# Optimization experiments

Hardware: AMD Instinct MI355X
Metric: run time of the kernel (lower is better)

## Reference

```python
import jax, jax.numpy as jnp
import numpy as np

N_NODES = 80000
N_EDGES = 1280000
N_GRAPHS = 256
NEG_SLOPE = 0.2


def _edge_softmax(alpha, dst, n):
    # PyG softmax over incoming edges per target node, with 1e-16 eps
    m = jax.ops.segment_max(alpha, dst, num_segments=n)          # [N,H]
    e = jnp.exp(alpha - m[dst])
    s = jax.ops.segment_sum(e, dst, num_segments=n)              # [N,H]
    return e / (s[dst] + 1e-16)


def _gat_layer(x, src, dst, W, a_src, a_dst, b, heads, out_ch):
    n = x.shape[0]
    h = (x @ W).reshape(n, heads, out_ch)                        # [N,H,C]
    al_src = (h * a_src).sum(-1)                                 # [N,H]
    al_dst = (h * a_dst).sum(-1)                                 # [N,H]
    alpha = jax.nn.leaky_relu(al_src[src] + al_dst[dst], NEG_SLOPE)  # [E,H]
    alpha = _edge_softmax(alpha, dst, n)
    out = jax.ops.segment_sum(h[src] * alpha[:, :, None], dst, num_segments=n)
    return out.reshape(n, heads * out_ch) + b


def setup_inputs() -> dict:
    key = jax.random.key(0)
    ks = jax.random.split(key, 16)
    x = jax.random.normal(ks[0], (N_NODES, 9), dtype=jnp.float32)
    edge_index = jax.random.randint(ks[1], (2, N_EDGES), 0, N_NODES, dtype=jnp.int64)
    batch = jnp.sort(jax.random.randint(ks[2], (N_NODES,), 0, N_GRAPHS, dtype=jnp.int64))
    s = 0.1
    p = {}
    p['W1'] = jax.random.normal(ks[3], (9, 3 * 45), dtype=jnp.float32) * s
    p['a_src1'] = jax.random.normal(ks[4], (3, 45), dtype=jnp.float32) * s
    p['a_dst1'] = jax.random.normal(ks[5], (3, 45), dtype=jnp.float32) * s
    p['b1'] = jnp.zeros((3 * 45,), dtype=jnp.float32)
    p['W2'] = jax.random.normal(ks[6], (135, 3 * 18), dtype=jnp.float32) * s
    p['a_src2'] = jax.random.normal(ks[7], (3, 18), dtype=jnp.float32) * s
    p['a_dst2'] = jax.random.normal(ks[8], (3, 18), dtype=jnp.float32) * s
    p['b2'] = jnp.zeros((3 * 18,), dtype=jnp.float32)
    p['W3'] = jax.random.normal(ks[9], (54, 4), dtype=jnp.float32) * s
    p['a_src3'] = jax.random.normal(ks[10], (1, 4), dtype=jnp.float32) * s
    p['a_dst3'] = jax.random.normal(ks[11], (1, 4), dtype=jnp.float32) * s
    p['b3'] = jnp.zeros((4,), dtype=jnp.float32)
    return dict(x=x, edge_index=edge_index, batch=batch, **p)


def reference(x, edge_index, batch,
              W1, a_src1, a_dst1, b1,
              W2, a_src2, a_dst2, b2,
              W3, a_src3, a_dst3, b3):
    n = x.shape[0]
    # GATConv default: add self-loops once (same structure every layer)
    loop = jnp.arange(n, dtype=edge_index.dtype)
    src = jnp.concatenate([edge_index[0], loop])
    dst = jnp.concatenate([edge_index[1], loop])

    h = _gat_layer(x, src, dst, W1, a_src1, a_dst1, b1, 3, 45)
    h = jax.nn.relu(h)  # dropout is identity in eval mode
    h = _gat_layer(h, src, dst, W2, a_src2, a_dst2, b2, 3, 18)
    h = jax.nn.relu(h)
    h = _gat_layer(h, src, dst, W3, a_src3, a_dst3, b3, 1, 4)

    g = jax.ops.segment_max(h, batch, num_segments=N_GRAPHS)  # global_max_pool
    g = jnp.where(jnp.isneginf(g), jnp.float32(-1e9), g)      # guard empty graphs
    return jax.nn.log_softmax(g, axis=1)
```

## Files before the change

### kernel.cpp

```cpp
#include <hip/hip_runtime.h>
#include <hip/hip_bf16.h>
#include <hip/hip_fp16.h>

#define N_NODES 80000
#define N_EDGES 1280000
#define E_TOT   (N_EDGES + N_NODES)
#define N_GRAPHS 256
#define NEG_SLOPE 0.2f

__device__ __forceinline__ float leaky(float a) { return fmaxf(a, NEG_SLOPE * a); }

template <int H>
__device__ __forceinline__ float pick(const float (&arr)[H], int h) {
    float r = arr[0];
    #pragma unroll
    for (int j = 1; j < H; ++j) r = (h == j) ? arr[j] : r;
    return r;
}

__device__ __forceinline__ unsigned f2mono(float f) {
    unsigned u = __float_as_uint(f);
    return u ^ ((u >> 31) ? 0xFFFFFFFFu : 0x80000000u);
}
__device__ __forceinline__ float mono2f(unsigned u) {
    u = (u & 0x80000000u) ? (u ^ 0x80000000u) : ~u;
    return __uint_as_float(u);
}

__global__ void k_init(int* __restrict__ counts, unsigned* __restrict__ genc) {
    int i = blockIdx.x * blockDim.x + threadIdx.x;
    if (i < N_NODES) counts[i] = 1;
    if (i < N_GRAPHS * 4) genc[i] = f2mono(-1e9f);
}

__global__ void k_hist(const int* __restrict__ dst, int* __restrict__ counts,
                       int* __restrict__ erank) {
    int i = blockIdx.x * blockDim.x + threadIdx.x;
    if (i >= N_EDGES) return;
    erank[i] = atomicAdd(&counts[dst[i]], 1);
}

#define SCAN_B 256
__global__ void k_scan_block(const int* __restrict__ counts, int* __restrict__ rp,
                             int* __restrict__ bsum, int n) {
    __shared__ int sa[SCAN_B], sb[SCAN_B];
    int tid = threadIdx.x;
    int gi = blockIdx.x * SCAN_B + tid;
    int v = (gi < n) ? counts[gi] : 0;
    sa[tid] = v;
    __syncthreads();
    int* cur = sa; int* nxt = sb;
    #pragma unroll
    for (int d = 1; d < SCAN_B; d <<= 1) {
        int t = cur[tid];
        if (tid >= d) t += cur[tid - d];
        nxt[tid] = t;
        __syncthreads();
        int* tmp = cur; cur = nxt; nxt = tmp;
    }
    if (gi < n) rp[gi] = cur[tid] - v;
    if (tid == SCAN_B - 1) bsum[blockIdx.x] = cur[tid];
}

__global__ void k_scan_tops(const int* __restrict__ bsum, int* __restrict__ boff, int nb) {
    __shared__ int sa[512], sb[512];
    int tid = threadIdx.x;
    int v = (tid < nb) ? bsum[tid] : 0;
    sa[tid] = v;
    __syncthreads();
    int* cur = sa; int* nxt = sb;
    #pragma unroll
    for (int d = 1; d < 512; d <<= 1) {
        int t = cur[tid];
        if (tid >= d) t += cur[tid - d];
        nxt[tid] = t;
        __syncthreads();
        int* tmp = cur; cur = nxt; nxt = tmp;
    }
    if (tid < nb) boff[tid] = cur[tid] - v;
}

__global__ void k_scan_add_pre1(int* __restrict__ rp, const int* __restrict__ boff,
                                int* __restrict__ srcs,
                                const float* __restrict__ x, const float* __restrict__ W1,
                                const float* __restrict__ as1, const float* __restrict__ ad1,
                                float* __restrict__ als, float* __restrict__ ald, int n) {
    __shared__ float ps[27], pd[27];
    int t = threadIdx.x;
    int gi = blockIdx.x * blockDim.x + t;
    if (gi < n) {
        int r = rp[gi] + boff[blockIdx.x];
        rp[gi] = r;
        srcs[r] = gi;
    }
    if (gi == 0) rp[n] = E_TOT;
    if (t < 27) {
        int h = t / 9, k = t % 9;
        float s = 0.f, d = 0.f;
        for (int c = 0; c < 45; ++c) {
            float w = W1[k * 135 + h * 45 + c];
            s += w * as1[h * 45 + c];
            d += w * ad1[h * 45 + c];
        }
        ps[t] = s; pd[t] = d;
    }
    __syncthreads();
    if (gi >= n) return;
    float xr[9];
    #pragma unroll
    for (int k = 0; k < 9; ++k) xr[k] = x[gi * 9 + k];
    #pragma unroll
    for (int h = 0; h < 3; ++h) {
        float s = 0.f, d = 0.f;
        #pragma unroll
        for (int k = 0; k < 9; ++k) { s += xr[k] * ps[h * 9 + k]; d += xr[k] * pd[h * 9 + k]; }
        als[gi * 3 + h] = s;
        ald[gi * 3 + h] = d;
    }
}

__global__ void k_scatter(const int* __restrict__ src, const int* __restrict__ dst,
                          const int* __restrict__ rp, const int* __restrict__ erank,
                          int* __restrict__ srcs) {
    int i = blockIdx.x * blockDim.x + threadIdx.x;
    if (i >= N_EDGES) return;
    srcs[rp[dst[i]] + erank[i]] = src[i];
}

__global__ void k_agg1x(const int* __restrict__ rp, const int* __restrict__ srcs,
                        const float* __restrict__ x, const float* __restrict__ als,
                        const float* __restrict__ ald, float* __restrict__ wv,
                        float* __restrict__ aggx, int n) {
    int wid = threadIdx.x >> 6, lane = threadIdx.x & 63;
    int node = blockIdx.x * (blockDim.x >> 6) + wid;
    if (node >= n) return;
    int beg = rp[node], end = rp[node + 1];

    float aldv[3];
    #pragma unroll
    for (int h = 0; h < 3; ++h) aldv[h] = ald[node * 3 + h];

    float ss[3] = {0.f, 0.f, 0.f};
    for (int i = beg + lane; i < end; i += 64) {
        int s = srcs[i];
        #pragma unroll
        for (int h = 0; h < 3; ++h) {
            float e = __expf(leaky(als[s * 3 + h] + aldv[h]));
            wv[i * 3 + h] = e;
            ss[h] += e;
        }
    }
    #pragma unroll
    for (int h = 0; h < 3; ++h) {
        #pragma unroll
        for (int off = 32; off; off >>= 1) ss[h] += __shfl_xor(ss[h], off, 64);
    }
    float inv[3];
    #pragma unroll
    for (int h = 0; h < 3; ++h) inv[h] = 1.f / (ss[h] + 1e-16f);

    int es = lane >> 5, li = lane & 31;
    int lic = li < 27 ? li : 26;
    int hh = lic / 9;
    int kk = lic % 9;
    float invh = pick(inv, hh);

    float acc = 0.f;
    int i = beg + es;
    for (; i + 14 < end; i += 16) {
        int s0 = srcs[i],      s1 = srcs[i + 2],  s2 = srcs[i + 4],  s3 = srcs[i + 6];
        int s4 = srcs[i + 8],  s5 = srcs[i + 10], s6 = srcs[i + 12], s7 = srcs[i + 14];
        float w0 = wv[i * 3 + hh],        w1 = wv[(i + 2) * 3 + hh];
        float w2 = wv[(i + 4) * 3 + hh],  w3 = wv[(i + 6) * 3 + hh];
        float w4 = wv[(i + 8) * 3 + hh],  w5 = wv[(i + 10) * 3 + hh];
        float w6 = wv[(i + 12) * 3 + hh], w7 = wv[(i + 14) * 3 + hh];
        float x0 = x[s0 * 9 + kk], x1 = x[s1 * 9 + kk];
        float x2 = x[s2 * 9 + kk], x3 = x[s3 * 9 + kk];
        float x4 = x[s4 * 9 + kk], x5 = x[s5 * 9 + kk];
        float x6 = x[s6 * 9 + kk], x7 = x[s7 * 9 + kk];
        acc += x0 * w0 + x1 * w1 + x2 * w2 + x3 * w3
             + x4 * w4 + x5 * w5 + x6 * w6 + x7 * w7;
    }
    for (; i < end; i += 2) {
        acc += x[srcs[i] * 9 + kk] * wv[i * 3 + hh];
    }
    acc += __shfl_xor(acc, 32, 64);
    if (lane < 27) aggx[node * 27 + lane] = acc * invh;
}

__global__ void k_lin2f(const float* __restrict__ aggx, const float* __restrict__ W1,
                        const float* __restrict__ b1, const float* __restrict__ W2,
                        const float* __restrict__ as2, const float* __restrict__ ad2,
                        __half2* __restrict__ h2, float* __restrict__ als,
                        float* __restrict__ ald, int n) {
    int node = blockIdx.x * blockDim.x + threadIdx.x;
    if (node >= n) return;
    float ax[27];
    #pragma unroll
    for (int j = 0; j < 27; ++j) ax[j] = aggx[node * 27 + j];
    float acc[54];
    #pragma unroll
    for (int c = 0; c < 54; ++c) acc[c] = 0.f;
    #pragma unroll
    for (int h = 0; h < 3; ++h) {
        #pragma unroll 1
        for (int c0 = 0; c0 < 45; ++c0) {
            int col = h * 45 + c0;
            float t = b1[col];
            #pragma unroll
            for (int k = 0; k < 9; ++k) t += ax[h * 9 + k] * W1[k * 135 + col];
            t = fmaxf(t, 0.f);
            #pragma unroll
            for (int cc = 0; cc < 54; ++cc) acc[cc] += t * W2[col * 54 + cc];
        }
    }
    float as_[3] = {0.f, 0.f, 0.f}, ad_[3] = {0.f, 0.f, 0.f};
    #pragma unroll
    for (int c = 0; c < 54; ++c) {
        as_[c / 18] += acc[c] * as2[c];
        ad_[c / 18] += acc[c] * ad2[c];
    }
    #pragma unroll
    for (int j = 0; j < 27; ++j)
        h2[node * 27 + j] = __floats2half2_rn(acc[2 * j], acc[2 * j + 1]);
    #pragma unroll
    for (int h = 0; h < 3; ++h) { als[node * 3 + h] = as_[h]; ald[node * 3 + h] = ad_[h]; }
}

__global__ void k_agg2(const int* __restrict__ rp, const int* __restrict__ srcs,
                       const __half2* __restrict__ hv, const float* __restrict__ als,
                       const float* __restrict__ ald, float* __restrict__ wv,
                       const float* __restrict__ bias, const float* __restrict__ W3,
                       const float* __restrict__ as3, const float* __restrict__ ad3,
                       float* __restrict__ h3, float* __restrict__ als3,
                       float* __restrict__ ald3, int n) {
    int wid = threadIdx.x >> 6, lane = threadIdx.x & 63;
    int node = blockIdx.x * (blockDim.x >> 6) + wid;
    if (node >= n) return;
    int beg = rp[node], end = rp[node + 1];

    float aldv[3];
    #pragma unroll
    for (int hh = 0; hh < 3; ++hh) aldv[hh] = ald[node * 3 + hh];

    float ss[3] = {0.f, 0.f, 0.f};
    for (int i = beg + lane; i < end; i += 64) {
        int s = srcs[i];
        #pragma unroll
        for (int hh = 0; hh < 3; ++hh) {
            float e = __expf(leaky(als[s * 3 + hh] + aldv[hh]));
            wv[i * 3 + hh] = e;
            ss[hh] += e;
        }
    }
    #pragma unroll
    for (int hh = 0; hh < 3; ++hh) {
        #pragma unroll
        for (int off = 32; off; off >>= 1) ss[hh] += __shfl_xor(ss[hh], off, 64);
    }
    float inv[3];
    #pragma unroll
    for (int hh = 0; hh < 3; ++hh) inv[hh] = 1.f / (ss[hh] + 1e-16f);

    int es = lane >> 5, li = lane & 31;
    bool act = li < 27;
    int lic = act ? li : 26;
    int hh = lic / 9;
    float invh = pick(inv, hh);

    float accx = 0.f, accy = 0.f;
    int i = beg + es;
    for (; i + 14 < end; i += 16) {
        int s0 = srcs[i],      s1 = srcs[i + 2],  s2 = srcs[i + 4],  s3 = srcs[i + 6];
        int s4 = srcs[i + 8],  s5 = srcs[i + 10], s6 = srcs[i + 12], s7 = srcs[i + 14];
        float w0 = wv[i * 3 + hh],        w1 = wv[(i + 2) * 3 + hh];
        float w2 = wv[(i + 4) * 3 + hh],  w3 = wv[(i + 6) * 3 + hh];
        float w4 = wv[(i + 8) * 3 + hh],  w5 = wv[(i + 10) * 3 + hh];
        float w6 = wv[(i + 12) * 3 + hh], w7 = wv[(i + 14) * 3 + hh];
        float2 v0 = __half22float2(hv[s0 * 27 + lic]), v1 = __half22float2(hv[s1 * 27 + lic]);
        float2 v2 = __half22float2(hv[s2 * 27 + lic]), v3 = __half22float2(hv[s3 * 27 + lic]);
        float2 v4 = __half22float2(hv[s4 * 27 + lic]), v5 = __half22float2(hv[s5 * 27 + lic]);
        float2 v6 = __half22float2(hv[s6 * 27 + lic]), v7 = __half22float2(hv[s7 * 27 + lic]);
        accx += v0.x * w0 + v1.x * w1 + v2.x * w2 + v3.x * w3
              + v4.x * w4 + v5.x * w5 + v6.x * w6 + v7.x * w7;
        accy += v0.y * w0 + v1.y * w1 + v2.y * w2 + v3.y * w3
              + v4.y * w4 + v5.y * w5 + v6.y * w6 + v7.y * w7;
    }
    for (; i < end; i += 2) {
        float w = wv[i * 3 + hh];
        float2 v = __half22float2(hv[srcs[i] * 27 + lic]);
        accx += v.x * w;
        accy += v.y * w;
    }
    accx += __shfl_xor(accx, 32, 64);
    accy += __shfl_xor(accy, 32, 64);

    float p0 = 0.f, p1 = 0.f, p2 = 0.f, p3 = 0.f;
    if (act) {
        float2 b = ((const float2*)bias)[lic];
        float r0 = fmaxf(accx * invh + b.x, 0.f);
        float r1 = fmaxf(accy * invh + b.y, 0.f);
        int c0 = 2 * lic, c1 = 2 * lic + 1;
        p0 = r0 * W3[c0 * 4 + 0] + r1 * W3[c1 * 4 + 0];
        p1 = r0 * W3[c0 * 4 + 1] + r1 * W3[c1 * 4 + 1];
        p2 = r0 * W3[c0 * 4 + 2] + r1 * W3[c1 * 4 + 2];
        p3 = r0 * W3[c0 * 4 + 3] + r1 * W3[c1 * 4 + 3];
    }
    #pragma unroll
    for (int off = 16; off; off >>= 1) {
        p0 += __shfl_xor(p0, off, 64);
        p1 += __shfl_xor(p1, off, 64);
        p2 += __shfl_xor(p2, off, 64);
        p3 += __shfl_xor(p3, off, 64);
    }
    if (lane == 0) {
        float4 o; o.x = p0; o.y = p1; o.z = p2; o.w = p3;
        ((float4*)h3)[node] = o;
        als3[node] = p0 * as3[0] + p1 * as3[1] + p2 * as3[2] + p3 * as3[3];
        ald3[node] = p0 * ad3[0] + p1 * ad3[1] + p2 * ad3[2] + p3 * ad3[3];
    }
}

__global__ void k_agg3pool(const int* __restrict__ rp, const int* __restrict__ srcs,
                           const float* __restrict__ h3, const float* __restrict__ als3,
                           const float* __restrict__ ald3, const float* __restrict__ b3,
                           const int* __restrict__ batch, unsigned* __restrict__ genc, int n) {
    int sub = threadIdx.x & 15;
    int node = blockIdx.x * (blockDim.x >> 4) + (threadIdx.x >> 4);
    if (node >= n) return;
    int beg = rp[node], end = rp[node + 1];
    float aldv = ald3[node];

    float ss = 0.f;
    for (int i = beg + sub; i < end; i += 16)
        ss += __expf(leaky(als3[srcs[i]] + aldv));
    #pragma unroll
    for (int off = 8; off; off >>= 1) ss += __shfl_xor(ss, off, 64);
    float inv = 1.f / (ss + 1e-16f);

    float ax = 0.f, ay = 0.f, az = 0.f, aw = 0.f;
    const float4* h4 = (const float4*)h3;
    for (int i = beg + sub; i < end; i += 16) {
        int s = srcs[i];
        float w = __expf(leaky(als3[s] + aldv));
        float4 v = h4[s];
        ax += v.x * w; ay += v.y * w; az += v.z * w; aw += v.w * w;
    }
    #pragma unroll
    for (int off = 8; off; off >>= 1) {
        ax += __shfl_xor(ax, off, 64);
        ay += __shfl_xor(ay, off, 64);
        az += __shfl_xor(az, off, 64);
        aw += __shfl_xor(aw, off, 64);
    }
    if (sub < 4) {
        float v = (sub == 0) ? ax : (sub == 1) ? ay : (sub == 2) ? az : aw;
        atomicMax(&genc[batch[node] * 4 + sub], f2mono(v * inv + b3[sub]));
    }
}

__global__ void k_final(const unsigned* __restrict__ genc, float* __restrict__ out) {
    int g = threadIdx.x;
    float v[4];
    #pragma unroll
    for (int c = 0; c < 4; ++c) v[c] = mono2f(genc[g * 4 + c]);
    float mx = fmaxf(fmaxf(v[0], v[1]), fmaxf(v[2], v[3]));
    float s = 0.f;
    #pragma unroll
    for (int c = 0; c < 4; ++c) s += expf(v[c] - mx);
    float l = mx + logf(s);
    #pragma unroll
    for (int c = 0; c < 4; ++c) out[g * 4 + c] = v[c] - l;
}

extern "C" void kernel_launch(void* const* d_in, const int* in_sizes, int n_in,
                              void* d_out, int out_size, void* d_ws, size_t ws_size,
                              hipStream_t stream) {
    const float* x     = (const float*)d_in[0];
    const int*   ei    = (const int*)d_in[1];
    const int*   batch = (const int*)d_in[2];
    const float* W1    = (const float*)d_in[3];
    const float* as1   = (const float*)d_in[4];
    const float* ad1   = (const float*)d_in[5];
    const float* b1    = (const float*)d_in[6];
    const float* W2    = (const float*)d_in[7];
    const float* as2   = (const float*)d_in[8];
    const float* ad2   = (const float*)d_in[9];
    const float* b2    = (const float*)d_in[10];
    const float* W3    = (const float*)d_in[11];
    const float* as3   = (const float*)d_in[12];
    const float* ad3   = (const float*)d_in[13];
    const float* b3    = (const float*)d_in[14];
    float* out = (float*)d_out;

    const int* src = ei;
    const int* dst = ei + N_EDGES;

    char* base = (char*)d_ws;
    size_t off = 0;
    auto alloc = [&](size_t bytes) -> char* {
        char* p = base + off;
        off = (off + bytes + 255) & ~(size_t)255;
        return p;
    };
    int*      counts  = (int*)alloc((size_t)N_NODES * 4);
    int*      row_ptr = (int*)alloc((size_t)(N_NODES + 1) * 4);
    int*      srcs    = (int*)alloc((size_t)E_TOT * 4);
    int*      erank   = (int*)alloc((size_t)N_EDGES * 4);
    int*      bsum    = (int*)alloc(512 * 4);
    int*      boff    = (int*)alloc(512 * 4);
    float*    als     = (float*)alloc((size_t)N_NODES * 3 * 4);
    float*    ald     = (float*)alloc((size_t)N_NODES * 3 * 4);
    float*    als3    = (float*)alloc((size_t)N_NODES * 4);
    float*    ald3    = (float*)alloc((size_t)N_NODES * 4);
    float*    wv      = (float*)alloc((size_t)E_TOT * 3 * 4);
    float*    aggx    = (float*)alloc((size_t)N_NODES * 27 * 4);
    __half2*  h2      = (__half2*)alloc((size_t)N_NODES * 27 * 4);
    float*    h3      = (float*)alloc((size_t)N_NODES * 4 * 4);
    unsigned* genc    = (unsigned*)alloc((size_t)N_GRAPHS * 4 * 4);
    if (off > ws_size) return;

    const int TB = 256;
    const int nb_n  = (N_NODES + TB - 1) / TB;
    const int nb_e  = (N_EDGES + TB - 1) / TB;
    const int nb_w  = (N_NODES + 3) / 4;
    const int nb_16 = (N_NODES + 15) / 16;

    k_init<<<nb_n, TB, 0, stream>>>(counts, genc);
    k_hist<<<nb_e, TB, 0, stream>>>(dst, counts, erank);
    k_scan_block<<<nb_n, SCAN_B, 0, stream>>>(counts, row_ptr, bsum, N_NODES);
    k_scan_tops<<<1, 512, 0, stream>>>(bsum, boff, nb_n);
    k_scan_add_pre1<<<nb_n, TB, 0, stream>>>(row_ptr, boff, srcs, x, W1, as1, ad1, als, ald, N_NODES);
    k_scatter<<<nb_e, TB, 0, stream>>>(src, dst, row_ptr, erank, srcs);

    k_agg1x<<<nb_w, TB, 0, stream>>>(row_ptr, srcs, x, als, ald, wv, aggx, N_NODES);

    k_lin2f<<<nb_n, TB, 0, stream>>>(aggx, W1, b1, W2, as2, ad2, h2, als, ald, N_NODES);
    k_agg2<<<nb_w, TB, 0, stream>>>(row_ptr, srcs, h2, als, ald, wv, b2,
                                    W3, as3, ad3, h3, als3, ald3, N_NODES);

    k_agg3pool<<<nb_16, TB, 0, stream>>>(row_ptr, srcs, h3, als3, ald3, b3, batch, genc, N_NODES);
    k_final<<<1, N_GRAPHS, 0, stream>>>(genc, out);
}
```

Measured before the change: 478.8 us.

## Fuse edge-softmax denominator into aggregation loop, drop per-edge weight buffer

The separate pass that computed exp weights, wrote them to a per-edge buffer and summed them is removed in all three aggregation kernels. Each lane now recomputes the exp weight inline in the gather loop, accumulates the softmax denominator alongside the weighted features, and normalizes at the end via shuffles. This cuts a full edge pass and the write and re-read of the weight buffer. In exchange the exp work is repeated per feature lane rather than once per edge and head.

```diff
diff --git a/kernel.cpp b/kernel.cpp
--- a/kernel.cpp
+++ b/kernel.cpp
@@ -129,8 +129,7 @@
 
 __global__ void k_agg1x(const int* __restrict__ rp, const int* __restrict__ srcs,
                         const float* __restrict__ x, const float* __restrict__ als,
-                        const float* __restrict__ ald, float* __restrict__ wv,
-                        float* __restrict__ aggx, int n) {
+                        const float* __restrict__ ald, float* __restrict__ aggx, int n) {
     int wid = threadIdx.x >> 6, lane = threadIdx.x & 63;
     int node = blockIdx.x * (blockDim.x >> 6) + wid;
     if (node >= n) return;
@@ -140,52 +139,43 @@
     #pragma unroll
     for (int h = 0; h < 3; ++h) aldv[h] = ald[node * 3 + h];
 
-    float ss[3] = {0.f, 0.f, 0.f};
-    for (int i = beg + lane; i < end; i += 64) {
-        int s = srcs[i];
-        #pragma unroll
-        for (int h = 0; h < 3; ++h) {
-            float e = __expf(leaky(als[s * 3 + h] + aldv[h]));
-            wv[i * 3 + h] = e;
-            ss[h] += e;
-        }
-    }
-    #pragma unroll
-    for (int h = 0; h < 3; ++h) {
-        #pragma unroll
-        for (int off = 32; off; off >>= 1) ss[h] += __shfl_xor(ss[h], off, 64);
-    }
-    float inv[3];
-    #pragma unroll
-    for (int h = 0; h < 3; ++h) inv[h] = 1.f / (ss[h] + 1e-16f);
-
     int es = lane >> 5, li = lane & 31;
     int lic = li < 27 ? li : 26;
     int hh = lic / 9;
     int kk = lic % 9;
-    float invh = pick(inv, hh);
-
-    float acc = 0.f;
+    float aldh = pick(aldv, hh);
+
+    float acc = 0.f, ssp = 0.f;
     int i = beg + es;
     for (; i + 14 < end; i += 16) {
         int s0 = srcs[i],      s1 = srcs[i + 2],  s2 = srcs[i + 4],  s3 = srcs[i + 6];
         int s4 = srcs[i + 8],  s5 = srcs[i + 10], s6 = srcs[i + 12], s7 = srcs[i + 14];
-        float w0 = wv[i * 3 + hh],        w1 = wv[(i + 2) * 3 + hh];
-        float w2 = wv[(i + 4) * 3 + hh],  w3 = wv[(i + 6) * 3 + hh];
-        float w4 = wv[(i + 8) * 3 + hh],  w5 = wv[(i + 10) * 3 + hh];
-        float w6 = wv[(i + 12) * 3 + hh], w7 = wv[(i + 14) * 3 + hh];
+        float a0 = als[s0 * 3 + hh], a1 = als[s1 * 3 + hh];
+        float a2 = als[s2 * 3 + hh], a3 = als[s3 * 3 + hh];
+        float a4 = als[s4 * 3 + hh], a5 = als[s5 * 3 + hh];
+        float a6 = als[s6 * 3 + hh], a7 = als[s7 * 3 + hh];
         float x0 = x[s0 * 9 + kk], x1 = x[s1 * 9 + kk];
         float x2 = x[s2 * 9 + kk], x3 = x[s3 * 9 + kk];
         float x4 = x[s4 * 9 + kk], x5 = x[s5 * 9 + kk];
         float x6 = x[s6 * 9 + kk], x7 = x[s7 * 9 + kk];
+        float w0 = __expf(leaky(a0 + aldh)), w1 = __expf(leaky(a1 + aldh));
+        float w2 = __expf(leaky(a2 + aldh)), w3 = __expf(leaky(a3 + aldh));
+        float w4 = __expf(leaky(a4 + aldh)), w5 = __expf(leaky(a5 + aldh));
+        float w6 = __expf(leaky(a6 + aldh)), w7 = __expf(leaky(a7 + aldh));
+        ssp += (w0 + w1 + w2 + w3) + (w4 + w5 + w6 + w7);
         acc += x0 * w0 + x1 * w1 + x2 * w2 + x3 * w3
              + x4 * w4 + x5 * w5 + x6 * w6 + x7 * w7;
     }
     for (; i < end; i += 2) {
-        acc += x[srcs[i] * 9 + kk] * wv[i * 3 + hh];
-    }
+        int s = srcs[i];
+        float w = __expf(leaky(als[s * 3 + hh] + aldh));
+        ssp += w;
+        acc += x[s * 9 + kk] * w;
+    }
+    float sst = __shfl(ssp, hh * 9, 64) + __shfl(ssp, 32 + hh * 9, 64);
+    float inv = 1.f / (sst + 1e-16f);
     acc += __shfl_xor(acc, 32, 64);
-    if (lane < 27) aggx[node * 27 + lane] = acc * invh;
+    if (lane < 27) aggx[node * 27 + lane] = acc * inv;
 }
 
 __global__ void k_lin2f(const float* __restrict__ aggx, const float* __restrict__ W1,
@@ -229,7 +219,7 @@
 
 __global__ void k_agg2(const int* __restrict__ rp, const int* __restrict__ srcs,
                        const __half2* __restrict__ hv, const float* __restrict__ als,
-                       const float* __restrict__ ald, float* __restrict__ wv,
+                       const float* __restrict__ ald,
                        const float* __restrict__ bias, const float* __restrict__ W3,
                        const float* __restrict__ as3, const float* __restrict__ ad3,
                        float* __restrict__ h3, float* __restrict__ als3,
@@ -243,55 +233,45 @@
     #pragma unroll
     for (int hh = 0; hh < 3; ++hh) aldv[hh] = ald[node * 3 + hh];
 
-    float ss[3] = {0.f, 0.f, 0.f};
-    for (int i = beg + lane; i < end; i += 64) {
-        int s = srcs[i];
-        #pragma unroll
-        for (int hh = 0; hh < 3; ++hh) {
-            float e = __expf(leaky(als[s * 3 + hh] + aldv[hh]));
-            wv[i * 3 + hh] = e;
-            ss[hh] += e;
-        }
-    }
-    #pragma unroll
-    for (int hh = 0; hh < 3; ++hh) {
-        #pragma unroll
-        for (int off = 32; off; off >>= 1) ss[hh] += __shfl_xor(ss[hh], off, 64);
-    }
-    float inv[3];
-    #pragma unroll
-    for (int hh = 0; hh < 3; ++hh) inv[hh] = 1.f / (ss[hh] + 1e-16f);
-
     int es = lane >> 5, li = lane & 31;
     bool act = li < 27;
     int lic = act ? li : 26;
     int hh = lic / 9;
-    float invh = pick(inv, hh);
-
-    float accx = 0.f, accy = 0.f;
+    float aldh = pick(aldv, hh);
+
+    float accx = 0.f, accy = 0.f, ssp = 0.f;
     int i = beg + es;
     for (; i + 14 < end; i += 16) {
         int s0 = srcs[i],      s1 = srcs[i + 2],  s2 = srcs[i + 4],  s3 = srcs[i + 6];
         int s4 = srcs[i + 8],  s5 = srcs[i + 10], s6 = srcs[i + 12], s7 = srcs[i + 14];
-        float w0 = wv[i * 3 + hh],        w1 = wv[(i + 2) * 3 + hh];
-        float w2 = wv[(i + 4) * 3 + hh],  w3 = wv[(i + 6) * 3 + hh];
-        float w4 = wv[(i + 8) * 3 + hh],  w5 = wv[(i + 10) * 3 + hh];
-        float w6 = wv[(i + 12) * 3 + hh], w7 = wv[(i + 14) * 3 + hh];
+        float a0 = als[s0 * 3 + hh], a1 = als[s1 * 3 + hh];
+        float a2 = als[s2 * 3 + hh], a3 = als[s3 * 3 + hh];
+        float a4 = als[s4 * 3 + hh], a5 = als[s5 * 3 + hh];
+        float a6 = als[s6 * 3 + hh], a7 = als[s7 * 3 + hh];
         float2 v0 = __half22float2(hv[s0 * 27 + lic]), v1 = __half22float2(hv[s1 * 27 + lic]);
         float2 v2 = __half22float2(hv[s2 * 27 + lic]), v3 = __half22float2(hv[s3 * 27 + lic]);
         float2 v4 = __half22float2(hv[s4 * 27 + lic]), v5 = __half22float2(hv[s5 * 27 + lic]);
         float2 v6 = __half22float2(hv[s6 * 27 + lic]), v7 = __half22float2(hv[s7 * 27 + lic]);
+        float w0 = __expf(leaky(a0 + aldh)), w1 = __expf(leaky(a1 + aldh));
+        float w2 = __expf(leaky(a2 + aldh)), w3 = __expf(leaky(a3 + aldh));
+        float w4 = __expf(leaky(a4 + aldh)), w5 = __expf(leaky(a5 + aldh));
+        float w6 = __expf(leaky(a6 + aldh)), w7 = __expf(leaky(a7 + aldh));
+        ssp += (w0 + w1 + w2 + w3) + (w4 + w5 + w6 + w7);
         accx += v0.x * w0 + v1.x * w1 + v2.x * w2 + v3.x * w3
               + v4.x * w4 + v5.x * w5 + v6.x * w6 + v7.x * w7;
         accy += v0.y * w0 + v1.y * w1 + v2.y * w2 + v3.y * w3
               + v4.y * w4 + v5.y * w5 + v6.y * w6 + v7.y * w7;
     }
     for (; i < end; i += 2) {
-        float w = wv[i * 3 + hh];
-        float2 v = __half22float2(hv[srcs[i] * 27 + lic]);
+        int s = srcs[i];
+        float w = __expf(leaky(als[s * 3 + hh] + aldh));
+        float2 v = __half22float2(hv[s * 27 + lic]);
+        ssp += w;
         accx += v.x * w;
         accy += v.y * w;
     }
+    float sst = __shfl(ssp, hh * 9, 64) + __shfl(ssp, 32 + hh * 9, 64);
+    float invh = 1.f / (sst + 1e-16f);
     accx += __shfl_xor(accx, 32, 64);
     accy += __shfl_xor(accy, 32, 64);
 
@@ -331,29 +311,25 @@
     int beg = rp[node], end = rp[node + 1];
     float aldv = ald3[node];
 
-    float ss = 0.f;
-    for (int i = beg + sub; i < end; i += 16)
-        ss += __expf(leaky(als3[srcs[i]] + aldv));
-    #pragma unroll
-    for (int off = 8; off; off >>= 1) ss += __shfl_xor(ss, off, 64);
-    float inv = 1.f / (ss + 1e-16f);
-
-    float ax = 0.f, ay = 0.f, az = 0.f, aw = 0.f;
+    float ss = 0.f, ax = 0.f, ay = 0.f, az = 0.f, aw = 0.f;
     const float4* h4 = (const float4*)h3;
     for (int i = beg + sub; i < end; i += 16) {
         int s = srcs[i];
         float w = __expf(leaky(als3[s] + aldv));
         float4 v = h4[s];
+        ss += w;
         ax += v.x * w; ay += v.y * w; az += v.z * w; aw += v.w * w;
     }
     #pragma unroll
     for (int off = 8; off; off >>= 1) {
+        ss += __shfl_xor(ss, off, 64);
         ax += __shfl_xor(ax, off, 64);
         ay += __shfl_xor(ay, off, 64);
         az += __shfl_xor(az, off, 64);
         aw += __shfl_xor(aw, off, 64);
     }
     if (sub < 4) {
+        float inv = 1.f / (ss + 1e-16f);
         float v = (sub == 0) ? ax : (sub == 1) ? ay : (sub == 2) ? az : aw;
         atomicMax(&genc[batch[node] * 4 + sub], f2mono(v * inv + b3[sub]));
     }
@@ -413,7 +389,6 @@
     float*    ald     = (float*)alloc((size_t)N_NODES * 3 * 4);
     float*    als3    = (float*)alloc((size_t)N_NODES * 4);
     float*    ald3    = (float*)alloc((size_t)N_NODES * 4);
-    float*    wv      = (float*)alloc((size_t)E_TOT * 3 * 4);
     float*    aggx    = (float*)alloc((size_t)N_NODES * 27 * 4);
     __half2*  h2      = (__half2*)alloc((size_t)N_NODES * 27 * 4);
     float*    h3      = (float*)alloc((size_t)N_NODES * 4 * 4);
@@ -433,10 +408,10 @@
     k_scan_add_pre1<<<nb_n, TB, 0, stream>>>(row_ptr, boff, srcs, x, W1, as1, ad1, als, ald, N_NODES);
     k_scatter<<<nb_e, TB, 0, stream>>>(src, dst, row_ptr, erank, srcs);
 
-    k_agg1x<<<nb_w, TB, 0, stream>>>(row_ptr, srcs, x, als, ald, wv, aggx, N_NODES);
+    k_agg1x<<<nb_w, TB, 0, stream>>>(row_ptr, srcs, x, als, ald, aggx, N_NODES);
 
     k_lin2f<<<nb_n, TB, 0, stream>>>(aggx, W1, b1, W2, as2, ad2, h2, als, ald, N_NODES);
-    k_agg2<<<nb_w, TB, 0, stream>>>(row_ptr, srcs, h2, als, ald, wv, b2,
+    k_agg2<<<nb_w, TB, 0, stream>>>(row_ptr, srcs, h2, als, ald, b2,
                                     W3, as3, ad3, h3, als3, ald3, N_NODES);
 
     k_agg3pool<<<nb_16, TB, 0, stream>>>(row_ptr, srcs, h3, als3, ald3, b3, batch, genc, N_NODES);
```

Result: faster. 442.2 us (-7.6%).
